# Optimization experiments

Measured on AMD Instinct MI355X. Metric: run time of the kernel, lower is better.

## Reference

```python
import jax, jax.numpy as jnp
import numpy as np

B, N, D, P = 32, 16, 64, 8  # batch, num_objs, in_feat_dim, patch size
PAIRS = N * (N - 1)


def _conv_relu(x, W, b):
    # Conv2d(kernel=3, stride=1, padding=1) + ReLU, NCHW/OIHW layout
    y = jax.lax.conv_general_dilated(
        x, W, window_strides=(1, 1), padding='SAME',
        dimension_numbers=('NCHW', 'OIHW', 'NCHW'))
    return jax.nn.relu(y + b[None, :, None, None])


def setup_inputs() -> dict:
    key = jax.random.key(0)
    ks = jax.random.split(key, 12)
    x = jax.random.normal(ks[0], (B, N, D, P, P), jnp.float32)
    # g_idx: cols 0,1 index into the repeated pair axis of size N*(N-1); col 2 is a 0/1 mask
    i0 = jax.random.randint(ks[1], (B, PAIRS, 1), 0, PAIRS)
    i1 = jax.random.randint(ks[2], (B, PAIRS, 1), 0, PAIRS)
    m = jax.random.randint(ks[3], (B, PAIRS, 1), 0, 2)
    g_idx = jnp.concatenate([i0, i1, m], axis=2)

    def w(k, o, i):
        return jax.random.normal(k, (o, i, 3, 3), jnp.float32) * (1.0 / np.sqrt(i * 9.0))

    return {
        'x': x, 'g_idx': g_idx,
        'W_rel': w(ks[4], D, 2 * D), 'b_rel': jnp.zeros((D,), jnp.float32),
        'W_self': w(ks[5], D, D), 'b_self': jnp.zeros((D,), jnp.float32),
        'W_aff': w(ks[6], D, D), 'b_aff': jnp.zeros((D,), jnp.float32),
        'W_agg': w(ks[7], D, 2 * D), 'b_agg': jnp.zeros((D,), jnp.float32),
    }


def reference(x, g_idx, W_rel, b_rel, W_self, b_self, W_aff, b_aff, W_agg, b_agg):
    b, n, d, p, _ = x.shape
    pairs = n * (n - 1)
    s = x
    # x1: [B, N*(N-1), D, P, P]
    x1 = jnp.tile(x, (1, n - 1, 1, 1, 1))

    def gather_pair(col):
        idx = g_idx[:, :, col][:, :, None, None, None]  # [B, pairs, 1, 1, 1]
        idx = jnp.broadcast_to(idx, (b, pairs, d, p, p))
        return jnp.take_along_axis(x1, idx, axis=1)

    y1 = gather_pair(0)
    y2 = gather_pair(1)
    mask = g_idx[:, :, 2][:, :, None, None, None].astype(x.dtype)
    r = jnp.concatenate([y1, y2], axis=2) * mask  # [B, pairs, 2D, P, P]
    r = _conv_relu(r.reshape(-1, 2 * d, p, p), W_rel, b_rel)
    r = r.reshape(b, n, n - 1, d, p, p).sum(axis=2)  # scatter-sum per object

    xs = _conv_relu(x.reshape(-1, d, p, p), W_self, b_self).reshape(b, n, d, p, p)
    pred = xs + r
    a = _conv_relu(pred.reshape(-1, d, p, p), W_aff, b_aff).reshape(b, n, d, p, p)
    a = jnp.concatenate([a, s], axis=2)  # [B, N, 2D, P, P]
    out = _conv_relu(a.reshape(-1, 2 * d, p, p), W_agg, b_agg).reshape(b, n, d, p, p)
    return out
```

## Files before the change

kernel.cpp:

```cpp
#include <hip/hip_runtime.h>


#define NIMG 512
#define IMGSZ 4096

using bf16x8 = __attribute__((ext_vector_type(8))) short;
using f32x4  = __attribute__((ext_vector_type(4))) float;
using u16x8  = __attribute__((ext_vector_type(8))) unsigned short;

__device__ inline unsigned short f2bf(float f) {
  union { float f; unsigned u; } v; v.f = f;
  unsigned r = v.u + 0x7fffu + ((v.u >> 16) & 1u);
  return (unsigned short)(r >> 16);
}

__device__ inline f32x4 bf4_to_f32(uint2 p) {
  union { unsigned u; float f; } c;
  f32x4 r;
  c.u = (p.x & 0xffffu) << 16;  r[0] = c.f;
  c.u = (p.x & 0xffff0000u);    r[1] = c.f;
  c.u = (p.y & 0xffffu) << 16;  r[2] = c.f;
  c.u = (p.y & 0xffff0000u);    r[3] = c.f;
  return r;
}

__global__ __launch_bounds__(256) void prep_w(
    const float* __restrict__ Wr, const float* __restrict__ Ws,
    const float* __restrict__ Wa, const float* __restrict__ Wg,
    unsigned short* __restrict__ Wt)
{
  int idx = blockIdx.x * 256 + threadIdx.x;
  if (idx >= 221184) return;
  float v;
  if (idx < 73728) {
    int c = idx / 36864, r = idx % 36864;
    int t = r >> 12, oc = (r >> 6) & 63, ic = r & 63;
    v = (c == 0 ? Ws : Wa)[oc * 576 + ic * 9 + t];
  } else {
    int r2 = idx - 73728;
    int half = r2 / 73728, rr = r2 % 73728;
    int t = rr >> 13, oc = (rr >> 7) & 63, ic = rr & 127;
    v = (half ? Wg : Wr)[oc * 1152 + ic * 9 + t];
  }
  Wt[idx] = f2bf(v);
}

__device__ inline void decode_img(int j, int& b, int& o) {
  b = ((j >> 7) << 3) | (j & 7);
  o = (j >> 3) & 15;
}

template<int ROWX>
__device__ inline void stage_x(const float* __restrict__ xb,
                               unsigned short* __restrict__ s,
                               int coff, int w, int px) {
#pragma unroll
  for (int r = 0; r < 8; ++r) {
    int ic0 = (w + 4 * r) * 2;
    const float* sp = xb + ic0 * 64;
    float a = sp[px], c = sp[64 + px];
    *(unsigned*)(s + px * ROWX + coff + ic0) =
        (unsigned)f2bf(a) | ((unsigned)f2bf(c) << 16);
  }
}

__global__ __launch_bounds__(256) void k1(
    const float* __restrict__ x,
    const unsigned short* __restrict__ Wt,
    unsigned short* __restrict__ cA, unsigned short* __restrict__ cB)
{
  constexpr int ROW = 72;
  __shared__ __align__(16) unsigned short sX[65 * ROW];
  int b, o;
  decode_img(blockIdx.x, b, o);
  const int img = b * 16 + o;
  const int tid = threadIdx.x;
  const int w = tid >> 6, lane = tid & 63;

  stage_x<ROW>(x + (size_t)img * IMGSZ, sX, 0, w, lane);
  if (tid < 36) ((unsigned*)(sX + 64 * ROW))[tid] = 0;
  __syncthreads();

  const int q = lane >> 4, n16 = lane & 15;
  const int ocb = w * 16;
  const int co = ocb + q * 4;

  int pyt[4], pxt[4];
#pragma unroll
  for (int t = 0; t < 4; ++t) { int p = t * 16 + n16; pyt[t] = p >> 3; pxt[t] = p & 7; }

  f32x4 aA[4] = {}, aB[4] = {};
  const unsigned short* WA = Wt + 73728 + (ocb + n16) * 128 + q * 8;
  const unsigned short* WB = WA + 64;
#pragma unroll
  for (int tap = 0; tap < 9; ++tap) {
    const int dy = tap / 3 - 1, dx = tap % 3 - 1;
    int spt[4];
#pragma unroll
    for (int t = 0; t < 4; ++t) {
      int sy = pyt[t] + dy, sx = pxt[t] + dx;
      spt[t] = ((unsigned)sy < 8u && (unsigned)sx < 8u) ? (sy * 8 + sx) : 64;
    }
#pragma unroll
    for (int ks = 0; ks < 2; ++ks) {
      bf16x8 aa = *(const bf16x8*)(WA + tap * 8192 + ks * 32);
      bf16x8 ab = *(const bf16x8*)(WB + tap * 8192 + ks * 32);
#pragma unroll
      for (int t = 0; t < 4; ++t) {
        bf16x8 bt = *(const bf16x8*)(sX + spt[t] * ROW + ks * 32 + q * 8);
        aA[t] = __builtin_amdgcn_mfma_f32_16x16x32_bf16(aa, bt, aA[t], 0, 0, 0);
        aB[t] = __builtin_amdgcn_mfma_f32_16x16x32_bf16(ab, bt, aB[t], 0, 0, 0);
      }
    }
  }

  const size_t ib = (size_t)img * IMGSZ;
#pragma unroll
  for (int t = 0; t < 4; ++t) {
    int p = t * 16 + n16;
    uint2 pa, pb;
    pa.x = (unsigned)f2bf(aA[t][0]) | ((unsigned)f2bf(aA[t][1]) << 16);
    pa.y = (unsigned)f2bf(aA[t][2]) | ((unsigned)f2bf(aA[t][3]) << 16);
    pb.x = (unsigned)f2bf(aB[t][0]) | ((unsigned)f2bf(aB[t][1]) << 16);
    pb.y = (unsigned)f2bf(aB[t][2]) | ((unsigned)f2bf(aB[t][3]) << 16);
    *(uint2*)(cA + ib + p * 64 + co) = pa;
    *(uint2*)(cB + ib + p * 64 + co) = pb;
  }
}

__global__ __launch_bounds__(256, 2) void k2(
    const float* __restrict__ x,
    const int* __restrict__ g_idx,
    const unsigned short* __restrict__ Wt,
    const float* __restrict__ b_rel, const float* __restrict__ b_self,
    const float* __restrict__ b_aff, const float* __restrict__ b_agg,
    const unsigned short* __restrict__ cA, const unsigned short* __restrict__ cB,
    float* __restrict__ out)
{
  constexpr int ROW = 72, ROW2 = 136, XROW = 68;
  __shared__ __align__(16) unsigned short sX[65 * ROW2];
  __shared__ __align__(16) unsigned short sPred[65 * ROW];
  __shared__ __align__(16) float sXS[64 * XROW];
  __shared__ int so1[15], so2[15];
  __shared__ float sm[15];

  int b, i;
  decode_img(blockIdx.x, b, i);
  const int img = b * 16 + i;
  const int tid = threadIdx.x;
  const int w = tid >> 6, lane = tid & 63;

  if (tid < 15) {
    const int* gp = g_idx + ((size_t)b * 240 + i * 15 + tid) * 3;
    so1[tid] = gp[0] & 15;
    so2[tid] = gp[1] & 15;
    sm[tid]  = (float)gp[2];
  }

  stage_x<ROW2>(x + (size_t)img * IMGSZ, sX, 64, w, lane);
  if (tid < 68) ((unsigned*)(sX + 64 * ROW2))[tid] = 0;
  if (tid < 36) ((unsigned*)(sPred + 64 * ROW))[tid] = 0;
  __syncthreads();

  const int q = lane >> 4, n16 = lane & 15;
  const int ocb = w * 16;
  const int co = ocb + q * 4;
  const int aw64  = (ocb + n16) * 64 + q * 8;
  const int aw128 = (ocb + n16) * 128 + q * 8;

  int pyt[4], pxt[4];
#pragma unroll
  for (int t = 0; t < 4; ++t) { int p = t * 16 + n16; pyt[t] = p >> 3; pxt[t] = p & 7; }

  {
    f32x4 f[4] = {};
    const unsigned short* WS = Wt + aw64;
#pragma unroll
    for (int tap = 0; tap < 9; ++tap) {
      const int dy = tap / 3 - 1, dx = tap % 3 - 1;
      int spt[4];
#pragma unroll
      for (int t = 0; t < 4; ++t) {
        int sy = pyt[t] + dy, sx = pxt[t] + dx;
        spt[t] = ((unsigned)sy < 8u && (unsigned)sx < 8u) ? (sy * 8 + sx) : 64;
      }
#pragma unroll
      for (int ks = 0; ks < 2; ++ks) {
        bf16x8 a = *(const bf16x8*)(WS + tap * 4096 + ks * 32);
#pragma unroll
        for (int t = 0; t < 4; ++t) {
          bf16x8 bt = *(const bf16x8*)(sX + spt[t] * ROW2 + 64 + ks * 32 + q * 8);
          f[t] = __builtin_amdgcn_mfma_f32_16x16x32_bf16(a, bt, f[t], 0, 0, 0);
        }
      }
    }
#pragma unroll
    for (int t = 0; t < 4; ++t) {
      int p = t * 16 + n16;
      f32x4 vs = f[t];
#pragma unroll
      for (int r = 0; r < 4; ++r) vs[r] = fmaxf(vs[r] + b_self[co + r], 0.f);
      *(f32x4*)(sXS + p * XROW + co) = vs;
    }
  }
  __syncthreads();

  {
    const size_t bb = (size_t)b * 16 * IMGSZ;
#pragma unroll 1
    for (int pass = 0; pass < 4; ++pass) {
      const int e = tid * 4 + pass * 1024;
      const int e_px = e >> 6, e_ic = e & 63;
      uint2 v1[15], v2[15];
#pragma unroll
      for (int j = 0; j < 15; ++j) {
        v1[j] = *(const uint2*)(cA + bb + (size_t)so1[j] * IMGSZ + e);
        v2[j] = *(const uint2*)(cB + bb + (size_t)so2[j] * IMGSZ + e);
      }
      f32x4 xv = *(const f32x4*)(sXS + e_px * XROW + e_ic);
      float acc[4], br[4];
#pragma unroll
      for (int r = 0; r < 4; ++r) { br[r] = b_rel[e_ic + r]; acc[r] = xv[r]; }
#pragma unroll
      for (int j = 0; j < 15; ++j) {
        float m = sm[j];
        f32x4 a1 = bf4_to_f32(v1[j]);
        f32x4 a2 = bf4_to_f32(v2[j]);
#pragma unroll
        for (int r = 0; r < 4; ++r)
          acc[r] += fmaxf(m * (a1[r] + a2[r]) + br[r], 0.f);
      }
      uint2 pk;
      pk.x = (unsigned)f2bf(acc[0]) | ((unsigned)f2bf(acc[1]) << 16);
      pk.y = (unsigned)f2bf(acc[2]) | ((unsigned)f2bf(acc[3]) << 16);
      *(uint2*)(sPred + e_px * ROW + e_ic) = pk;
    }
  }
  __syncthreads();

  {
    f32x4 f[4] = {};
    const unsigned short* WA = Wt + 36864 + aw64;
#pragma unroll
    for (int tap = 0; tap < 9; ++tap) {
      const int dy = tap / 3 - 1, dx = tap % 3 - 1;
      int spt[4];
#pragma unroll
      for (int t = 0; t < 4; ++t) {
        int sy = pyt[t] + dy, sx = pxt[t] + dx;
        spt[t] = ((unsigned)sy < 8u && (unsigned)sx < 8u) ? (sy * 8 + sx) : 64;
      }
#pragma unroll
      for (int ks = 0; ks < 2; ++ks) {
        bf16x8 a = *(const bf16x8*)(WA + tap * 4096 + ks * 32);
#pragma unroll
        for (int t = 0; t < 4; ++t) {
          bf16x8 bt = *(const bf16x8*)(sPred + spt[t] * ROW + ks * 32 + q * 8);
          f[t] = __builtin_amdgcn_mfma_f32_16x16x32_bf16(a, bt, f[t], 0, 0, 0);
        }
      }
    }
#pragma unroll
    for (int t = 0; t < 4; ++t) {
      int p = t * 16 + n16;
      float v0 = fmaxf(f[t][0] + b_aff[co + 0], 0.f);
      float v1 = fmaxf(f[t][1] + b_aff[co + 1], 0.f);
      float v2 = fmaxf(f[t][2] + b_aff[co + 2], 0.f);
      float v3 = fmaxf(f[t][3] + b_aff[co + 3], 0.f);
      uint2 pk;
      pk.x = (unsigned)f2bf(v0) | ((unsigned)f2bf(v1) << 16);
      pk.y = (unsigned)f2bf(v2) | ((unsigned)f2bf(v3) << 16);
      *(uint2*)(sX + p * ROW2 + co) = pk;
    }
  }
  __syncthreads();

  {
    f32x4 g[4] = {};
    const unsigned short* WG = Wt + 147456 + aw128;
#pragma unroll
    for (int tap = 0; tap < 9; ++tap) {
      const int dy = tap / 3 - 1, dx = tap % 3 - 1;
      int spt[4];
#pragma unroll
      for (int t = 0; t < 4; ++t) {
        int sy = pyt[t] + dy, sx = pxt[t] + dx;
        spt[t] = ((unsigned)sy < 8u && (unsigned)sx < 8u) ? (sy * 8 + sx) : 64;
      }
#pragma unroll
      for (int ks = 0; ks < 4; ++ks) {
        bf16x8 a = *(const bf16x8*)(WG + tap * 8192 + ks * 32);
#pragma unroll
        for (int t = 0; t < 4; ++t) {
          bf16x8 bt = *(const bf16x8*)(sX + spt[t] * ROW2 + ks * 32 + q * 8);
          g[t] = __builtin_amdgcn_mfma_f32_16x16x32_bf16(a, bt, g[t], 0, 0, 0);
        }
      }
    }
    float* ob = out + (size_t)img * IMGSZ;
#pragma unroll
    for (int t = 0; t < 4; ++t) {
      int p = t * 16 + n16;
#pragma unroll
      for (int r = 0; r < 4; ++r)
        ob[(co + r) * 64 + p] = fmaxf(g[t][r] + b_agg[co + r], 0.f);
    }
  }
}

extern "C" void kernel_launch(void* const* d_in, const int* in_sizes, int n_in,
                              void* d_out, int out_size, void* d_ws, size_t ws_size,
                              hipStream_t stream) {
  const float* x      = (const float*)d_in[0];
  const int*   g_idx  = (const int*)  d_in[1];
  const float* W_rel  = (const float*)d_in[2];
  const float* b_rel  = (const float*)d_in[3];
  const float* W_self = (const float*)d_in[4];
  const float* b_self = (const float*)d_in[5];
  const float* W_aff  = (const float*)d_in[6];
  const float* b_aff  = (const float*)d_in[7];
  const float* W_agg  = (const float*)d_in[8];
  const float* b_agg  = (const float*)d_in[9];
  float* out = (float*)d_out;

  unsigned short* cA = (unsigned short*)d_ws;
  unsigned short* cB = cA + 2097152;
  unsigned short* Wt = cB + 2097152;

  prep_w<<<864, 256, 0, stream>>>(W_rel, W_self, W_aff, W_agg, Wt);
  k1<<<NIMG, 256, 0, stream>>>(x, Wt, cA, cB);
  k2<<<NIMG, 256, 0, stream>>>(x, g_idx, Wt, b_rel, b_self, b_aff, b_agg,
                               cA, cB, out);
}
```

Measured before the change: 118.4 us.

## Fuse k1 and k2 into one cooperative kernel with per-batch counter sync

Merges the two conv kernels into a single cooperatively launched kernel. Each block writes its pair-conv partials, then raises a per-batch atomic counter. While the other blocks of that batch finish, it computes the self conv, and it spin-waits until all 16 blocks of the batch are done before gathering. This removes a kernel launch boundary and overlaps the self conv with the cross-block dependency, at the cost of spin-wait latency and needing all 512 blocks co-resident (2 per CU). It falls back to the two-kernel path if the cooperative launch fails.

```diff
diff --git a/kernel.cpp b/kernel.cpp
--- a/kernel.cpp
+++ b/kernel.cpp
@@ -6,7 +6,6 @@
 
 using bf16x8 = __attribute__((ext_vector_type(8))) short;
 using f32x4  = __attribute__((ext_vector_type(4))) float;
-using u16x8  = __attribute__((ext_vector_type(8))) unsigned short;
 
 __device__ inline unsigned short f2bf(float f) {
   union { float f; unsigned u; } v; v.f = f;
@@ -27,8 +26,9 @@
 __global__ __launch_bounds__(256) void prep_w(
     const float* __restrict__ Wr, const float* __restrict__ Ws,
     const float* __restrict__ Wa, const float* __restrict__ Wg,
-    unsigned short* __restrict__ Wt)
+    unsigned short* __restrict__ Wt, int* __restrict__ cnt)
 {
+  if (blockIdx.x == 0 && threadIdx.x < 32) cnt[threadIdx.x * 32] = 0;
   int idx = blockIdx.x * 256 + threadIdx.x;
   if (idx >= 221184) return;
   float v;
@@ -61,6 +61,239 @@
     float a = sp[px], c = sp[64 + px];
     *(unsigned*)(s + px * ROWX + coff + ic0) =
         (unsigned)f2bf(a) | ((unsigned)f2bf(c) << 16);
+  }
+}
+
+__global__ __launch_bounds__(256, 2) void kfused(
+    const float* __restrict__ x,
+    const int* __restrict__ g_idx,
+    const unsigned short* __restrict__ Wt,
+    const float* __restrict__ b_rel, const float* __restrict__ b_self,
+    const float* __restrict__ b_aff, const float* __restrict__ b_agg,
+    unsigned short* __restrict__ cA, unsigned short* __restrict__ cB,
+    int* __restrict__ cnt,
+    float* __restrict__ out)
+{
+  constexpr int ROW = 72, ROW2 = 136, XROW = 68;
+  __shared__ __align__(16) unsigned short sX[65 * ROW2];
+  __shared__ __align__(16) unsigned short sPred[65 * ROW];
+  __shared__ __align__(16) float sXS[64 * XROW];
+  __shared__ int so1[15], so2[15];
+  __shared__ float sm[15];
+
+  int b, i;
+  decode_img(blockIdx.x, b, i);
+  const int img = b * 16 + i;
+  const int tid = threadIdx.x;
+  const int w = tid >> 6, lane = tid & 63;
+  const int b32 = b * 32;
+
+  if (tid < 15) {
+    const int* gp = g_idx + ((size_t)b * 240 + i * 15 + tid) * 3;
+    so1[tid] = gp[0] & 15;
+    so2[tid] = gp[1] & 15;
+    sm[tid]  = (float)gp[2];
+  }
+
+  stage_x<ROW2>(x + (size_t)img * IMGSZ, sX, 64, w, lane);
+  if (tid < 68) ((unsigned*)(sX + 64 * ROW2))[tid] = 0;
+  if (tid < 36) ((unsigned*)(sPred + 64 * ROW))[tid] = 0;
+  __syncthreads();
+
+  const int q = lane >> 4, n16 = lane & 15;
+  const int ocb = w * 16;
+  const int co = ocb + q * 4;
+  const int aw64  = (ocb + n16) * 64 + q * 8;
+  const int aw128 = (ocb + n16) * 128 + q * 8;
+
+  int pyt[4], pxt[4];
+#pragma unroll
+  for (int t = 0; t < 4; ++t) { int p = t * 16 + n16; pyt[t] = p >> 3; pxt[t] = p & 7; }
+
+  {
+    f32x4 aA[4] = {}, aB[4] = {};
+    const unsigned short* WA = Wt + 73728 + aw128;
+    const unsigned short* WB = WA + 64;
+#pragma unroll
+    for (int tap = 0; tap < 9; ++tap) {
+      const int dy = tap / 3 - 1, dx = tap % 3 - 1;
+      int spt[4];
+#pragma unroll
+      for (int t = 0; t < 4; ++t) {
+        int sy = pyt[t] + dy, sx = pxt[t] + dx;
+        spt[t] = ((unsigned)sy < 8u && (unsigned)sx < 8u) ? (sy * 8 + sx) : 64;
+      }
+#pragma unroll
+      for (int ks = 0; ks < 2; ++ks) {
+        bf16x8 aa = *(const bf16x8*)(WA + tap * 8192 + ks * 32);
+        bf16x8 ab = *(const bf16x8*)(WB + tap * 8192 + ks * 32);
+#pragma unroll
+        for (int t = 0; t < 4; ++t) {
+          bf16x8 bt = *(const bf16x8*)(sX + spt[t] * ROW2 + 64 + ks * 32 + q * 8);
+          aA[t] = __builtin_amdgcn_mfma_f32_16x16x32_bf16(aa, bt, aA[t], 0, 0, 0);
+          aB[t] = __builtin_amdgcn_mfma_f32_16x16x32_bf16(ab, bt, aB[t], 0, 0, 0);
+        }
+      }
+    }
+    const size_t ib = (size_t)img * IMGSZ;
+#pragma unroll
+    for (int t = 0; t < 4; ++t) {
+      int p = t * 16 + n16;
+      uint2 pa, pb;
+      pa.x = (unsigned)f2bf(aA[t][0]) | ((unsigned)f2bf(aA[t][1]) << 16);
+      pa.y = (unsigned)f2bf(aA[t][2]) | ((unsigned)f2bf(aA[t][3]) << 16);
+      pb.x = (unsigned)f2bf(aB[t][0]) | ((unsigned)f2bf(aB[t][1]) << 16);
+      pb.y = (unsigned)f2bf(aB[t][2]) | ((unsigned)f2bf(aB[t][3]) << 16);
+      *(uint2*)(cA + ib + p * 64 + co) = pa;
+      *(uint2*)(cB + ib + p * 64 + co) = pb;
+    }
+  }
+
+  __threadfence();
+  __syncthreads();
+  if (tid == 0)
+    __hip_atomic_fetch_add(cnt + b32, 1, __ATOMIC_RELEASE, __HIP_MEMORY_SCOPE_AGENT);
+
+  {
+    f32x4 f[4] = {};
+    const unsigned short* WS = Wt + aw64;
+#pragma unroll
+    for (int tap = 0; tap < 9; ++tap) {
+      const int dy = tap / 3 - 1, dx = tap % 3 - 1;
+      int spt[4];
+#pragma unroll
+      for (int t = 0; t < 4; ++t) {
+        int sy = pyt[t] + dy, sx = pxt[t] + dx;
+        spt[t] = ((unsigned)sy < 8u && (unsigned)sx < 8u) ? (sy * 8 + sx) : 64;
+      }
+#pragma unroll
+      for (int ks = 0; ks < 2; ++ks) {
+        bf16x8 a = *(const bf16x8*)(WS + tap * 4096 + ks * 32);
+#pragma unroll
+        for (int t = 0; t < 4; ++t) {
+          bf16x8 bt = *(const bf16x8*)(sX + spt[t] * ROW2 + 64 + ks * 32 + q * 8);
+          f[t] = __builtin_amdgcn_mfma_f32_16x16x32_bf16(a, bt, f[t], 0, 0, 0);
+        }
+      }
+    }
+#pragma unroll
+    for (int t = 0; t < 4; ++t) {
+      int p = t * 16 + n16;
+      f32x4 vs = f[t];
+#pragma unroll
+      for (int r = 0; r < 4; ++r) vs[r] = fmaxf(vs[r] + b_self[co + r], 0.f);
+      *(f32x4*)(sXS + p * XROW + co) = vs;
+    }
+  }
+
+  if (tid == 0) {
+    while (__hip_atomic_load(cnt + b32, __ATOMIC_ACQUIRE, __HIP_MEMORY_SCOPE_AGENT) < 16)
+      __builtin_amdgcn_s_sleep(2);
+  }
+  __syncthreads();
+  __threadfence();
+
+  {
+    const size_t bb = (size_t)b * 16 * IMGSZ;
+#pragma unroll 1
+    for (int pass = 0; pass < 4; ++pass) {
+      const int e = tid * 4 + pass * 1024;
+      const int e_px = e >> 6, e_ic = e & 63;
+      uint2 v1[15], v2[15];
+#pragma unroll
+      for (int j = 0; j < 15; ++j) {
+        v1[j] = *(const uint2*)(cA + bb + (size_t)so1[j] * IMGSZ + e);
+        v2[j] = *(const uint2*)(cB + bb + (size_t)so2[j] * IMGSZ + e);
+      }
+      f32x4 xv = *(const f32x4*)(sXS + e_px * XROW + e_ic);
+      float acc[4], br[4];
+#pragma unroll
+      for (int r = 0; r < 4; ++r) { br[r] = b_rel[e_ic + r]; acc[r] = xv[r]; }
+#pragma unroll
+      for (int j = 0; j < 15; ++j) {
+        float m = sm[j];
+        f32x4 a1 = bf4_to_f32(v1[j]);
+        f32x4 a2 = bf4_to_f32(v2[j]);
+#pragma unroll
+        for (int r = 0; r < 4; ++r)
+          acc[r] += fmaxf(m * (a1[r] + a2[r]) + br[r], 0.f);
+      }
+      uint2 pk;
+      pk.x = (unsigned)f2bf(acc[0]) | ((unsigned)f2bf(acc[1]) << 16);
+      pk.y = (unsigned)f2bf(acc[2]) | ((unsigned)f2bf(acc[3]) << 16);
+      *(uint2*)(sPred + e_px * ROW + e_ic) = pk;
+    }
+  }
+  __syncthreads();
+
+  {
+    f32x4 f[4] = {};
+    const unsigned short* WA = Wt + 36864 + aw64;
+#pragma unroll
+    for (int tap = 0; tap < 9; ++tap) {
+      const int dy = tap / 3 - 1, dx = tap % 3 - 1;
+      int spt[4];
+#pragma unroll
+      for (int t = 0; t < 4; ++t) {
+        int sy = pyt[t] + dy, sx = pxt[t] + dx;
+        spt[t] = ((unsigned)sy < 8u && (unsigned)sx < 8u) ? (sy * 8 + sx) : 64;
+      }
+#pragma unroll
+      for (int ks = 0; ks < 2; ++ks) {
+        bf16x8 a = *(const bf16x8*)(WA + tap * 4096 + ks * 32);
+#pragma unroll
+        for (int t = 0; t < 4; ++t) {
+          bf16x8 bt = *(const bf16x8*)(sPred + spt[t] * ROW + ks * 32 + q * 8);
+          f[t] = __builtin_amdgcn_mfma_f32_16x16x32_bf16(a, bt, f[t], 0, 0, 0);
+        }
+      }
+    }
+#pragma unroll
+    for (int t = 0; t < 4; ++t) {
+      int p = t * 16 + n16;
+      float v0 = fmaxf(f[t][0] + b_aff[co + 0], 0.f);
+      float v1 = fmaxf(f[t][1] + b_aff[co + 1], 0.f);
+      float v2 = fmaxf(f[t][2] + b_aff[co + 2], 0.f);
+      float v3 = fmaxf(f[t][3] + b_aff[co + 3], 0.f);
+      uint2 pk;
+      pk.x = (unsigned)f2bf(v0) | ((unsigned)f2bf(v1) << 16);
+      pk.y = (unsigned)f2bf(v2) | ((unsigned)f2bf(v3) << 16);
+      *(uint2*)(sX + p * ROW2 + co) = pk;
+    }
+  }
+  __syncthreads();
+
+  {
+    f32x4 g[4] = {};
+    const unsigned short* WG = Wt + 147456 + aw128;
+#pragma unroll
+    for (int tap = 0; tap < 9; ++tap) {
+      const int dy = tap / 3 - 1, dx = tap % 3 - 1;
+      int spt[4];
+#pragma unroll
+      for (int t = 0; t < 4; ++t) {
+        int sy = pyt[t] + dy, sx = pxt[t] + dx;
+        spt[t] = ((unsigned)sy < 8u && (unsigned)sx < 8u) ? (sy * 8 + sx) : 64;
+      }
+#pragma unroll
+      for (int ks = 0; ks < 4; ++ks) {
+        bf16x8 a = *(const bf16x8*)(WG + tap * 8192 + ks * 32);
+#pragma unroll
+        for (int t = 0; t < 4; ++t) {
+          bf16x8 bt = *(const bf16x8*)(sX + spt[t] * ROW2 + ks * 32 + q * 8);
+          g[t] = __builtin_amdgcn_mfma_f32_16x16x32_bf16(bt, a, g[t], 0, 0, 0);
+        }
+      }
+    }
+    float* ob = out + (size_t)img * IMGSZ;
+    const float bg = b_agg[ocb + n16];
+#pragma unroll
+    for (int t = 0; t < 4; ++t) {
+      f32x4 v;
+#pragma unroll
+      for (int r = 0; r < 4; ++r) v[r] = fmaxf(g[t][r] + bg, 0.f);
+      *(f32x4*)(ob + (ocb + n16) * 64 + t * 16 + q * 4) = v;
+    }
   }
 }
 
@@ -326,9 +559,18 @@
   unsigned short* cA = (unsigned short*)d_ws;
   unsigned short* cB = cA + 2097152;
   unsigned short* Wt = cB + 2097152;
-
-  prep_w<<<864, 256, 0, stream>>>(W_rel, W_self, W_aff, W_agg, Wt);
-  k1<<<NIMG, 256, 0, stream>>>(x, Wt, cA, cB);
-  k2<<<NIMG, 256, 0, stream>>>(x, g_idx, Wt, b_rel, b_self, b_aff, b_agg,
-                               cA, cB, out);
-}
+  int* cnt = (int*)(Wt + 221184);
+
+  prep_w<<<864, 256, 0, stream>>>(W_rel, W_self, W_aff, W_agg, Wt, cnt);
+
+  void* args[] = {(void*)&x, (void*)&g_idx, (void*)&Wt, (void*)&b_rel,
+                  (void*)&b_self, (void*)&b_aff, (void*)&b_agg,
+                  (void*)&cA, (void*)&cB, (void*)&cnt, (void*)&out};
+  hipError_t ce = hipLaunchCooperativeKernel(
+      reinterpret_cast<void*>(kfused), dim3(NIMG), dim3(256), args, 0, stream);
+  if (ce != hipSuccess) {
+    k1<<<NIMG, 256, 0, stream>>>(x, Wt, cA, cB);
+    k2<<<NIMG, 256, 0, stream>>>(x, g_idx, Wt, b_rel, b_self, b_aff, b_agg,
+                                 cA, cB, out);
+  }
+}
```

Result: slower. 255.6 us (+115.9%).

## Compact masked pairs to skip zero-mask gathers and vectorize output stores

Applied to the files above, without the earlier changes.

A wave ballot compacts the per-object pair list to the pairs whose mask is nonzero. The relation accumulation then loads and sums only those pairs, in chunks of four. Masked-out pairs are folded in analytically as (15-na)*relu(bias), which removes about half of the gathered global loads from cA and cB. The final aggregation MFMA swaps its operands so each lane holds four consecutive pixels of one channel, letting the output be written with 16-byte vector stores instead of scalar strided stores. The trade-off is a data-dependent loop trip count with less unrolled load-level parallelism per chunk.

```diff
diff --git a/kernel.cpp b/kernel.cpp
--- a/kernel.cpp
+++ b/kernel.cpp
@@ -6,7 +6,6 @@
 
 using bf16x8 = __attribute__((ext_vector_type(8))) short;
 using f32x4  = __attribute__((ext_vector_type(4))) float;
-using u16x8  = __attribute__((ext_vector_type(8))) unsigned short;
 
 __device__ inline unsigned short f2bf(float f) {
   union { float f; unsigned u; } v; v.f = f;
@@ -141,8 +140,9 @@
   __shared__ __align__(16) unsigned short sX[65 * ROW2];
   __shared__ __align__(16) unsigned short sPred[65 * ROW];
   __shared__ __align__(16) float sXS[64 * XROW];
-  __shared__ int so1[15], so2[15];
-  __shared__ float sm[15];
+  __shared__ int so1a[16], so2a[16];
+  __shared__ float sma[16];
+  __shared__ int s_na;
 
   int b, i;
   decode_img(blockIdx.x, b, i);
@@ -150,11 +150,19 @@
   const int tid = threadIdx.x;
   const int w = tid >> 6, lane = tid & 63;
 
+  int o1v = 0, o2v = 0, mv = 0;
   if (tid < 15) {
     const int* gp = g_idx + ((size_t)b * 240 + i * 15 + tid) * 3;
-    so1[tid] = gp[0] & 15;
-    so2[tid] = gp[1] & 15;
-    sm[tid]  = (float)gp[2];
+    o1v = gp[0] & 15;
+    o2v = gp[1] & 15;
+    mv  = gp[2];
+  }
+  if (tid < 64) {
+    if (tid < 16) { so1a[tid] = 0; so2a[tid] = 0; sma[tid] = 0.f; }
+    unsigned long long mk = __ballot(mv != 0);
+    int pfx = (int)__popcll(mk & ((1ull << tid) - 1));
+    if (mv) { so1a[pfx] = o1v; so2a[pfx] = o2v; sma[pfx] = 1.f; }
+    if (tid == 0) s_na = (int)__popcll(mk);
   }
 
   stage_x<ROW2>(x + (size_t)img * IMGSZ, sX, 64, w, lane);
@@ -207,28 +215,38 @@
 
   {
     const size_t bb = (size_t)b * 16 * IMGSZ;
+    const int na = s_na;
+    const int nc = (na + 3) >> 2;
+    const float c0 = (float)(15 - na);
 #pragma unroll 1
     for (int pass = 0; pass < 4; ++pass) {
       const int e = tid * 4 + pass * 1024;
       const int e_px = e >> 6, e_ic = e & 63;
-      uint2 v1[15], v2[15];
-#pragma unroll
-      for (int j = 0; j < 15; ++j) {
-        v1[j] = *(const uint2*)(cA + bb + (size_t)so1[j] * IMGSZ + e);
-        v2[j] = *(const uint2*)(cB + bb + (size_t)so2[j] * IMGSZ + e);
-      }
       f32x4 xv = *(const f32x4*)(sXS + e_px * XROW + e_ic);
       float acc[4], br[4];
 #pragma unroll
-      for (int r = 0; r < 4; ++r) { br[r] = b_rel[e_ic + r]; acc[r] = xv[r]; }
-#pragma unroll
-      for (int j = 0; j < 15; ++j) {
-        float m = sm[j];
-        f32x4 a1 = bf4_to_f32(v1[j]);
-        f32x4 a2 = bf4_to_f32(v2[j]);
-#pragma unroll
-        for (int r = 0; r < 4; ++r)
-          acc[r] += fmaxf(m * (a1[r] + a2[r]) + br[r], 0.f);
+      for (int r = 0; r < 4; ++r) {
+        br[r] = b_rel[e_ic + r];
+        acc[r] = xv[r] + c0 * fmaxf(br[r], 0.f);
+      }
+#pragma unroll 1
+      for (int c = 0; c < nc; ++c) {
+        uint2 v1[4], v2[4];
+#pragma unroll
+        for (int jj = 0; jj < 4; ++jj) {
+          int j = c * 4 + jj;
+          v1[jj] = *(const uint2*)(cA + bb + (size_t)so1a[j] * IMGSZ + e);
+          v2[jj] = *(const uint2*)(cB + bb + (size_t)so2a[j] * IMGSZ + e);
+        }
+#pragma unroll
+        for (int jj = 0; jj < 4; ++jj) {
+          float s = sma[c * 4 + jj];
+          f32x4 a1 = bf4_to_f32(v1[jj]);
+          f32x4 a2 = bf4_to_f32(v2[jj]);
+#pragma unroll
+          for (int r = 0; r < 4; ++r)
+            acc[r] += s * fmaxf(a1[r] + a2[r] + br[r], 0.f);
+        }
       }
       uint2 pk;
       pk.x = (unsigned)f2bf(acc[0]) | ((unsigned)f2bf(acc[1]) << 16);
@@ -293,17 +311,18 @@
 #pragma unroll
         for (int t = 0; t < 4; ++t) {
           bf16x8 bt = *(const bf16x8*)(sX + spt[t] * ROW2 + ks * 32 + q * 8);
-          g[t] = __builtin_amdgcn_mfma_f32_16x16x32_bf16(a, bt, g[t], 0, 0, 0);
+          g[t] = __builtin_amdgcn_mfma_f32_16x16x32_bf16(bt, a, g[t], 0, 0, 0);
         }
       }
     }
     float* ob = out + (size_t)img * IMGSZ;
+    const float bg = b_agg[ocb + n16];
 #pragma unroll
     for (int t = 0; t < 4; ++t) {
-      int p = t * 16 + n16;
-#pragma unroll
-      for (int r = 0; r < 4; ++r)
-        ob[(co + r) * 64 + p] = fmaxf(g[t][r] + b_agg[co + r], 0.f);
+      f32x4 v;
+#pragma unroll
+      for (int r = 0; r < 4; ++r) v[r] = fmaxf(g[t][r] + bg, 0.f);
+      *(f32x4*)(ob + (ocb + n16) * 64 + t * 16 + q * 4) = v;
     }
   }
 }
```

Result: no change. 117.4 us (-0.9%).
